# Performance work log

Hardware: AMD Instinct MI355X
Metric: run time of the kernel (lower is better)

The kernel has to match this reference:

```python
import jax, jax.numpy as jnp
import numpy as np

K = 3        # ksize
S = 2        # stride_1
P = K // 2   # padding
SCALE = 10.0 # softmax_scale


def conv1x1(x, w, bias):
    # x: [bs, C, D, H, W], w: [O, C] (1x1x1 Conv3d), bias: [O]
    return jnp.einsum('bcdhw,oc->bodhw', x, w) + bias[None, :, None, None, None]


def _win_idx(n_in):
    n_out = (n_in + 2 * P - K) // S + 1
    idx = (jnp.arange(n_out) * S)[:, None] + jnp.arange(K)  # [n_out, K]
    return idx, n_out


def unfold2d(x):
    # x: [bs, C, H, W] -> patches [bs, C, nH, nW, K, K] (torch Unfold semantics, zero pad)
    bs, C, H, W = x.shape
    xp = jnp.pad(x, ((0, 0), (0, 0), (P, P), (P, P)))
    ri, nH = _win_idx(H)
    ci, nW = _win_idx(W)
    return xp[:, :, ri[:, None, :, None], ci[None, :, None, :]]


def fold2d(pat, H, W):
    # pat: [bs, C, nH, nW, K, K] -> [bs, C, H, W] via overlap-add (torch Fold)
    bs, C, nH, nW, _, _ = pat.shape
    ri, _ = _win_idx(H)
    ci, _ = _win_idx(W)
    out = jnp.zeros((bs, C, H + 2 * P, W + 2 * P), pat.dtype)
    out = out.at[:, :, ri[:, None, :, None], ci[None, :, None, :]].add(pat)
    return out[:, :, P:P + H, P:P + W]


def _patches_flat(x2d):
    # x2d: [bs, Ci, H, W] -> ([bs*L, Ci*K*K], nH, nW)  matching torch's
    # unfold -> view(bs,Ci,K,K,L) -> permute(0,4,1,2,3) -> reshape layout
    pat = unfold2d(x2d)                      # [bs, Ci, nH, nW, K, K]
    bs, Ci, nH, nW = pat.shape[:4]
    flat = jnp.transpose(pat, (0, 2, 3, 1, 4, 5)).reshape(bs * nH * nW, Ci * K * K)
    return flat, nH, nW


def salsa_one(b_one, g_w, g_b, th_w, th_b, ph_w, ph_b, W_w, W_b):
    bs, C, D, H, W = b_one.shape
    Ci = g_w.shape[0]
    b1 = conv1x1(b_one, g_w, g_b)    # query source
    b2 = conv1x1(b_one, th_w, th_b)  # value source
    b3 = conv1x1(b_one, ph_w, ph_b)  # key source
    mid = D // 2

    q, nH, nW = _patches_flat(b1[:, :, mid])   # [bs*L, Ci*K*K]
    v, _, _ = _patches_flat(b2[:, :, mid])
    kq, _, _ = _patches_flat(b3[:, :, mid])

    att = jax.nn.softmax(SCALE * (q @ kq.T), axis=1)  # [bs*L, bs*L]
    zi = att @ v                                      # [bs*L, Ci*K*K]

    pat = jnp.transpose(zi.reshape(bs, nH, nW, Ci, K, K), (0, 3, 1, 2, 4, 5))
    zi2 = fold2d(pat, H, W)                           # [bs, Ci, H, W]
    # overlap-count normalization: fold(unfold(ones))
    mask = fold2d(unfold2d(jnp.ones((bs, Ci, H, W), b_one.dtype)), H, W)
    zi2 = zi2 / mask

    zi5 = jnp.broadcast_to(zi2[:, :, None], (bs, Ci, D, H, W))
    return b_one + conv1x1(zi5, W_w, W_b)


def setup_inputs() -> dict:
    key = jax.random.key(0)
    ks = jax.random.split(key, 9)
    C, Ci = 64, 16
    b = jax.random.normal(ks[0], (2, 1, C, 8, 160, 160), dtype=jnp.float32)
    mk = lambda k, shp: jax.random.normal(k, shp, dtype=jnp.float32) * 0.05
    return {
        'b': b,
        'g_w': mk(ks[1], (Ci, C)), 'g_b': mk(ks[2], (Ci,)),
        'theta_w': mk(ks[3], (Ci, C)), 'theta_b': mk(ks[4], (Ci,)),
        'phi_w': mk(ks[5], (Ci, C)), 'phi_b': mk(ks[6], (Ci,)),
        'W_w': mk(ks[7], (C, Ci)), 'W_b': mk(ks[8], (C,)),
    }


def reference(b, g_w, g_b, theta_w, theta_b, phi_w, phi_b, W_w, W_b):
    f = lambda x: salsa_one(x, g_w, g_b, theta_w, theta_b, phi_w, phi_b, W_w, W_b)
    return jax.vmap(f)(b)
```

## Files before the change

### kernel.cpp

```cpp
#include <hip/hip_runtime.h>


#define NPIX 25600
#define LOG2E10 14.42695040888963f
#define TAU 0.75f

typedef float floatx16 __attribute__((ext_vector_type(16)));
typedef short short8 __attribute__((ext_vector_type(8)));

__device__ inline unsigned short f2bf(float x) {
    union { float f; unsigned int u; } v; v.f = x;
    unsigned int r = v.u + 0x7fffu + ((v.u >> 16) & 1u);
    return (unsigned short)(r >> 16);
}
__device__ inline float bf2f(unsigned short u) {
    union { unsigned int u; float f; } v; v.u = ((unsigned int)u) << 16;
    return v.f;
}

__global__ __launch_bounds__(256) void k_proj(
    const float* __restrict__ b,
    const float* __restrict__ gw, const float* __restrict__ gb,
    const float* __restrict__ thw, const float* __restrict__ thb,
    const float* __restrict__ phw, const float* __restrict__ phb,
    float* __restrict__ P3) {
    __shared__ float Wt[3 * 64 * 16];
    __shared__ float Bl[48];
    __shared__ float red[2][48][64];
    int tid = threadIdx.x;
    int g = blockIdx.y;
    int px = tid & 63;
    int cq = tid >> 6;
    int pix = blockIdx.x * 64 + px;

    for (int i = tid; i < 1024; i += 256) {
        int o = i & 15, c = i >> 4;
        Wt[(0 * 64 + c) * 16 + o] = gw[o * 64 + c];
        Wt[(1 * 64 + c) * 16 + o] = phw[o * 64 + c];
        Wt[(2 * 64 + c) * 16 + o] = thw[o * 64 + c];
    }
    if (tid < 16) { Bl[tid] = gb[tid]; Bl[16 + tid] = phb[tid]; Bl[32 + tid] = thb[tid]; }
    __syncthreads();

    float acc[48];
#pragma unroll
    for (int o = 0; o < 48; o++) acc[o] = 0.f;
    const float* bp = b + (size_t)g * 64 * 8 * NPIX + (size_t)4 * NPIX + pix;
#pragma unroll
    for (int i = 0; i < 16; i++) {
        int c = cq * 16 + i;
        float xv = bp[(size_t)c * 8 * NPIX];
#pragma unroll
        for (int s = 0; s < 3; s++) {
            const float* wp = &Wt[(s * 64 + c) * 16];
#pragma unroll
            for (int o = 0; o < 16; o++)
                acc[s * 16 + o] += wp[o] * xv;
        }
    }
    if (cq >= 2) {
#pragma unroll
        for (int o = 0; o < 48; o++) red[cq - 2][o][px] = acc[o];
    }
    __syncthreads();
    if (cq < 2) {
#pragma unroll
        for (int o = 0; o < 48; o++) acc[o] += red[cq][o][px];
    }
    __syncthreads();
    if (cq == 1) {
#pragma unroll
        for (int o = 0; o < 48; o++) red[0][o][px] = acc[o];
    }
    __syncthreads();
    if (cq == 0) {
#pragma unroll
        for (int o = 0; o < 48; o++)
            P3[(size_t)(g * 48 + o) * NPIX + pix] = acc[o] + red[0][o][px] + Bl[o];
    }
}

__global__ void k_unfold_qk(const float* __restrict__ P3, unsigned short* __restrict__ Pat) {
    int idx = blockIdx.x * 256 + threadIdx.x;
    int f = idx % 144;
    int l = (idx / 144) % 6400;
    int s = (idx / (144 * 6400)) & 1;
    int g = idx / (2 * 144 * 6400);
    int ci = f / 9, kr = (f % 9) / 3, kc = f % 3;
    int oh = l / 80, ow = l % 80;
    int h = oh * 2 + kr - 1, w = ow * 2 + kc - 1;
    float v = 0.f;
    if (h >= 0 && h < 160 && w >= 0 && w < 160)
        v = P3[(size_t)(g * 48 + s * 16 + ci) * NPIX + h * 160 + w];
    Pat[idx] = f2bf(v);
}

__global__ void k_unfold_v(const float* __restrict__ P3, unsigned short* __restrict__ VT) {
    int idx = blockIdx.x * 256 + threadIdx.x;
    int l = idx % 6400;
    int f = (idx / 6400) % 144;
    int g = idx / (144 * 6400);
    int ci = f / 9, kr = (f % 9) / 3, kc = f % 3;
    int oh = l / 80, ow = l % 80;
    int h = oh * 2 + kr - 1, w = ow * 2 + kc - 1;
    float v = 0.f;
    if (h >= 0 && h < 160 && w >= 0 && w < 160)
        v = P3[(size_t)(g * 48 + 32 + ci) * NPIX + h * 160 + w];
    VT[idx] = f2bf(v);
}

__global__ __launch_bounds__(256, 2) void k_attn(
    const unsigned short* __restrict__ PatQK, const unsigned short* __restrict__ VT,
    float* __restrict__ ml, unsigned short* __restrict__ Opart,
    int nsplit, int kps) {
    __shared__ unsigned short Ks[64 * 156];
    __shared__ unsigned short Vs[160 * 76];
    __shared__ unsigned short Pl[4 * 32 * 76];

    int tid = threadIdx.x;
    int lane = tid & 63;
    int w = tid >> 6;
    int l31 = lane & 31;
    int h5 = lane >> 5;
    int split = blockIdx.y, g = blockIdx.z;
    int q = blockIdx.x * 128 + w * 32 + l31;
    int nIter = kps >> 6;

    const unsigned short* Qg = PatQK + ((size_t)g * 2 + 0) * 6400 * 144;
    const unsigned short* Kg = PatQK + ((size_t)g * 2 + 1) * 6400 * 144 + (size_t)split * kps * 144;
    const unsigned short* Vg = VT + (size_t)g * 144 * 6400 + split * kps;

    short8 qf[9];
#pragma unroll
    for (int fs = 0; fs < 9; fs++)
        qf[fs] = *(const short8*)(Qg + (size_t)q * 144 + fs * 16 + h5 * 8);

    floatx16 O[5];
#pragma unroll
    for (int i = 0; i < 5; i++) O[i] = (floatx16)0.f;
    float m = -1e30f, lsum = 0.f;

    unsigned short* Plw = Pl + w * (32 * 76);

    short8 stg[9];
    {
#pragma unroll
        for (int j = 0; j < 9; j++) {
            int c = tid + 256 * j;
            if (c < 1152) {
                int row = c / 18, col = c - row * 18;
                stg[j] = *(const short8*)(Kg + row * 144 + col * 8);
            } else {
                int vv = c - 1152;
                int f = vv >> 3, col = vv & 7;
                stg[j] = *(const short8*)(Vg + (size_t)f * 6400 + col * 8);
            }
        }
#pragma unroll
        for (int j = 0; j < 9; j++) {
            int c = tid + 256 * j;
            if (c < 1152) {
                int row = c / 18, col = c - row * 18;
                *(short8*)&Ks[row * 156 + col * 8] = stg[j];
            } else {
                int vv = c - 1152;
                int f = vv >> 3, col = vv & 7;
                *(short8*)&Vs[f * 76 + col * 8] = stg[j];
            }
        }
    }

    for (int it = 0; it < nIter; it++) {
        __syncthreads();

        if (it + 1 < nIter) {
            const unsigned short* Kt = Kg + (it + 1) * 64 * 144;
            const unsigned short* Vt = Vg + (it + 1) * 64;
#pragma unroll
            for (int j = 0; j < 9; j++) {
                int c = tid + 256 * j;
                if (c < 1152) {
                    int row = c / 18, col = c - row * 18;
                    stg[j] = *(const short8*)(Kt + row * 144 + col * 8);
                } else {
                    int vv = c - 1152;
                    int f = vv >> 3, col = vv & 7;
                    stg[j] = *(const short8*)(Vt + (size_t)f * 6400 + col * 8);
                }
            }
        }

        floatx16 S0 = (floatx16)0.f, S1 = (floatx16)0.f;
#pragma unroll
        for (int fs = 0; fs < 9; fs++) {
            short8 a0 = *(const short8*)&Ks[l31 * 156 + fs * 16 + h5 * 8];
            short8 a1 = *(const short8*)&Ks[(32 + l31) * 156 + fs * 16 + h5 * 8];
            S0 = __builtin_amdgcn_mfma_f32_32x32x16_bf16(a0, qf[fs], S0, 0, 0, 0);
            S1 = __builtin_amdgcn_mfma_f32_32x32x16_bf16(a1, qf[fs], S1, 0, 0, 0);
        }

        float mt = -1e30f;
#pragma unroll
        for (int r = 0; r < 16; r++) { mt = fmaxf(mt, S0[r]); mt = fmaxf(mt, S1[r]); }
        mt = fmaxf(mt, __shfl_xor(mt, 32, 64));
        bool upd = mt > m + TAU;
        float mnew = upd ? mt : m;
        float alpha = upd ? exp2f(LOG2E10 * (m - mnew)) : 1.f;
        float ps = 0.f;
#pragma unroll
        for (int r = 0; r < 16; r++) {
            S0[r] = exp2f(LOG2E10 * (S0[r] - mnew));
            S1[r] = exp2f(LOG2E10 * (S1[r] - mnew));
            ps += S0[r] + S1[r];
        }
        ps += __shfl_xor(ps, 32, 64);
        lsum = lsum * alpha + ps;
        m = mnew;
        if (__any(alpha < 1.f)) {
#pragma unroll
            for (int t5 = 0; t5 < 5; t5++)
#pragma unroll
                for (int r = 0; r < 16; r++) O[t5][r] *= alpha;
        }

#pragma unroll
        for (int rg = 0; rg < 4; rg++) {
            ushort4 w0, w1;
            w0.x = f2bf(S0[4 * rg + 0]); w0.y = f2bf(S0[4 * rg + 1]);
            w0.z = f2bf(S0[4 * rg + 2]); w0.w = f2bf(S0[4 * rg + 3]);
            w1.x = f2bf(S1[4 * rg + 0]); w1.y = f2bf(S1[4 * rg + 1]);
            w1.z = f2bf(S1[4 * rg + 2]); w1.w = f2bf(S1[4 * rg + 3]);
            *(ushort4*)&Plw[l31 * 76 + rg * 8 + h5 * 4] = w0;
            *(ushort4*)&Plw[l31 * 76 + 32 + rg * 8 + h5 * 4] = w1;
        }

#pragma unroll
        for (int ks = 0; ks < 4; ks++) {
            short8 pb = *(const short8*)&Plw[l31 * 76 + ks * 16 + h5 * 8];
#pragma unroll
            for (int ft = 0; ft < 5; ft++) {
                short8 va = *(const short8*)&Vs[(ft * 32 + l31) * 76 + ks * 16 + h5 * 8];
                O[ft] = __builtin_amdgcn_mfma_f32_32x32x16_bf16(va, pb, O[ft], 0, 0, 0);
            }
        }

        __syncthreads();
        if (it + 1 < nIter) {
#pragma unroll
            for (int j = 0; j < 9; j++) {
                int c = tid + 256 * j;
                if (c < 1152) {
                    int row = c / 18, col = c - row * 18;
                    *(short8*)&Ks[row * 156 + col * 8] = stg[j];
                } else {
                    int vv = c - 1152;
                    int f = vv >> 3, col = vv & 7;
                    *(short8*)&Vs[f * 76 + col * 8] = stg[j];
                }
            }
        }
    }

    if (h5 == 0)
        ((float2*)ml)[((size_t)g * nsplit + split) * 6400 + q] = make_float2(m, lsum);

    unsigned short* Og = Opart + (((size_t)g * nsplit + split) * 6400 + q) * 144;
#pragma unroll
    for (int ft = 0; ft < 5; ft++)
#pragma unroll
        for (int rg = 0; rg < 4; rg++) {
            int f = ft * 32 + rg * 8 + h5 * 4;
            if (f < 144) {
                ushort4 st;
                st.x = f2bf(O[ft][4 * rg + 0]); st.y = f2bf(O[ft][4 * rg + 1]);
                st.z = f2bf(O[ft][4 * rg + 2]); st.w = f2bf(O[ft][4 * rg + 3]);
                *(ushort4*)(Og + f) = st;
            }
        }
}

__global__ void k_merge(const float* __restrict__ mlp, const unsigned short* __restrict__ Opart,
                        float* __restrict__ Zi, int nsplit) {
    int idx = blockIdx.x * 256 + threadIdx.x;
    int fg = idx % 36;
    int q = (idx / 36) % 6400;
    int g = idx / (36 * 6400);
    const float2* ml2 = (const float2*)mlp;
    float2 s[5];
    float ms = -1e30f;
#pragma unroll
    for (int k = 0; k < 5; k++) {
        s[k] = (k < nsplit) ? ml2[((size_t)g * nsplit + k) * 6400 + q]
                            : make_float2(-1e30f, 0.f);
        ms = fmaxf(ms, s[k].x);
    }
    float wgt[5], denom = 0.f;
#pragma unroll
    for (int k = 0; k < 5; k++) {
        wgt[k] = exp2f(LOG2E10 * (s[k].x - ms));
        denom += wgt[k] * s[k].y;
    }
    float inv = 1.f / denom;
    float a0 = 0.f, a1 = 0.f, a2 = 0.f, a3 = 0.f;
#pragma unroll
    for (int k = 0; k < 5; k++) {
        if (k < nsplit) {
            ushort4 u = *(const ushort4*)(Opart + (((size_t)g * nsplit + k) * 6400 + q) * 144 + fg * 4);
            a0 += wgt[k] * bf2f(u.x); a1 += wgt[k] * bf2f(u.y);
            a2 += wgt[k] * bf2f(u.z); a3 += wgt[k] * bf2f(u.w);
        }
    }
    float4 out = make_float4(a0 * inv, a1 * inv, a2 * inv, a3 * inv);
    *(float4*)(Zi + ((size_t)g * 6400 + q) * 144 + fg * 4) = out;
}

__global__ void k_fold(const float* __restrict__ Zi, float* __restrict__ zi2) {
    int idx = blockIdx.x * 256 + threadIdx.x;
    int pix = idx % NPIX;
    int ci = (idx / NPIX) & 15;
    int g = idx / (16 * NPIX);
    int h = pix / 160, w = pix % 160;
    int ohs[2], krs[2], nh = 0;
#pragma unroll
    for (int kr = 0; kr < 3; kr++) {
        int t = h + 1 - kr;
        if (t >= 0 && (t & 1) == 0 && (t >> 1) < 80) { ohs[nh] = t >> 1; krs[nh] = kr; nh++; }
    }
    int ows[2], kcs[2], nw = 0;
#pragma unroll
    for (int kc = 0; kc < 3; kc++) {
        int t = w + 1 - kc;
        if (t >= 0 && (t & 1) == 0 && (t >> 1) < 80) { ows[nw] = t >> 1; kcs[nw] = kc; nw++; }
    }
    float sm = 0.f;
    for (int a = 0; a < nh; a++)
        for (int bb = 0; bb < nw; bb++) {
            int l = ohs[a] * 80 + ows[bb];
            int f = ci * 9 + krs[a] * 3 + kcs[bb];
            sm += Zi[((size_t)g * 6400 + l) * 144 + f];
        }
    zi2[idx] = sm / (float)(nh * nw);
}

__global__ void k_final(const float* __restrict__ b, const float* __restrict__ zi2,
                        const float* __restrict__ Ww, const float* __restrict__ Wb,
                        float* __restrict__ out) {
    __shared__ float z[16 * 64];
    __shared__ float Wl[64 * 16];
    __shared__ float Bl[64];
    int tid = threadIdx.x;
    int g = blockIdx.y;
    int pxb = blockIdx.x * 64;
    for (int i = tid; i < 1024; i += 256) {
        int ci = i >> 6, px = i & 63;
        z[i] = zi2[(size_t)(g * 16 + ci) * NPIX + pxb + px];
        Wl[i] = Ww[i];
    }
    if (tid < 64) Bl[tid] = Wb[tid];
    __syncthreads();

    int px4 = tid & 15;
    int cg = tid >> 4;
    float acc[4][4];
#pragma unroll
    for (int c4 = 0; c4 < 4; c4++) {
        float bv = Bl[cg + 16 * c4];
#pragma unroll
        for (int j = 0; j < 4; j++) acc[c4][j] = bv;
    }
#pragma unroll
    for (int ci = 0; ci < 16; ci++) {
        float zv[4];
#pragma unroll
        for (int j = 0; j < 4; j++) zv[j] = z[ci * 64 + px4 * 4 + j];
#pragma unroll
        for (int c4 = 0; c4 < 4; c4++) {
            float wv = Wl[(cg + 16 * c4) * 16 + ci];
#pragma unroll
            for (int j = 0; j < 4; j++) acc[c4][j] += wv * zv[j];
        }
    }
    for (int d = 0; d < 8; d++) {
#pragma unroll
        for (int c4 = 0; c4 < 4; c4++) {
            int c = cg + 16 * c4;
            size_t base = ((size_t)(g * 64 + c) * 8 + d) * NPIX + pxb + px4 * 4;
            float4 bv = *(const float4*)(b + base);
            float4 ov = make_float4(bv.x + acc[c4][0], bv.y + acc[c4][1],
                                    bv.z + acc[c4][2], bv.w + acc[c4][3]);
            *(float4*)(out + base) = ov;
        }
    }
}

extern "C" void kernel_launch(void* const* d_in, const int* in_sizes, int n_in,
                              void* d_out, int out_size, void* d_ws, size_t ws_size,
                              hipStream_t stream) {
    const float* b   = (const float*)d_in[0];
    const float* gw  = (const float*)d_in[1];
    const float* gb  = (const float*)d_in[2];
    const float* thw = (const float*)d_in[3];
    const float* thb = (const float*)d_in[4];
    const float* phw = (const float*)d_in[5];
    const float* phb = (const float*)d_in[6];
    const float* Ww  = (const float*)d_in[7];
    const float* Wb  = (const float*)d_in[8];
    float* out = (float*)d_out;
    float* ws = (float*)d_ws;

    const size_t need5 = 30003200;
    int ns = (ws_size >= need5) ? 5 : 4;
    int kps = 6400 / ns;

    unsigned short* PatQK = (unsigned short*)ws;
    unsigned short* VT    = (unsigned short*)(ws + 1843200);
    float*          ml    = ws + 2764800;
    size_t off_P3 = 2764800 + (size_t)2 * ns * 6400 * 2;
    float*          P3    = ws + off_P3;
    unsigned short* Opart = (unsigned short*)(ws + off_P3);
    float*          Zi    = ws;
    float*          zi2   = ws + 1843200;

    k_proj<<<dim3(400, 2), 256, 0, stream>>>(b, gw, gb, thw, thb, phw, phb, P3);
    k_unfold_qk<<<dim3(14400), 256, 0, stream>>>(P3, PatQK);
    k_unfold_v<<<dim3(7200), 256, 0, stream>>>(P3, VT);
    k_attn<<<dim3(50, ns, 2), 256, 0, stream>>>(PatQK, VT, ml, Opart, ns, kps);
    k_merge<<<dim3(1800), 256, 0, stream>>>(ml, Opart, Zi, ns);
    k_fold<<<dim3(3200), 256, 0, stream>>>(Zi, zi2);
    k_final<<<dim3(400, 2), 256, 0, stream>>>(b, zi2, Ww, Wb, out);
}
```

Before: 344.0 us.

## Shrink attention LDS footprint, alias P buffer over K, raise occupancy and splits

The attention kernel now keeps K and V in one shared buffer with tighter padding, and reuses the K region for the per-wave probability tile. This needs an extra barrier after the score computation. Launch bounds ask for 4 blocks per CU instead of 2, and the key dimension is split 10 ways when the workspace allows it, with the merge kernel extended to match. The aim is more resident waves and more blocks to hide latency. The costs are register pressure that may cause spills, an extra sync per iteration, more partial outputs to merge, and possible bank conflicts from the new strides.

```diff
diff --git a/kernel.cpp b/kernel.cpp
--- a/kernel.cpp
+++ b/kernel.cpp
@@ -4,6 +4,12 @@
 #define NPIX 25600
 #define LOG2E10 14.42695040888963f
 #define TAU 0.75f
+
+#define KS_LD 146
+#define VS_LD 66
+#define PL_LD 66
+#define KS_SH (64 * KS_LD)
+#define VS_SH (160 * VS_LD)
 
 typedef float floatx16 __attribute__((ext_vector_type(16)));
 typedef short short8 __attribute__((ext_vector_type(8)));
@@ -109,13 +115,14 @@
     VT[idx] = f2bf(v);
 }
 
-__global__ __launch_bounds__(256, 2) void k_attn(
+__global__ __launch_bounds__(256, 4) void k_attn(
     const unsigned short* __restrict__ PatQK, const unsigned short* __restrict__ VT,
     float* __restrict__ ml, unsigned short* __restrict__ Opart,
     int nsplit, int kps) {
-    __shared__ unsigned short Ks[64 * 156];
-    __shared__ unsigned short Vs[160 * 76];
-    __shared__ unsigned short Pl[4 * 32 * 76];
+    __shared__ unsigned short SM[KS_SH + VS_SH];
+    unsigned short* Ks = SM;
+    unsigned short* Vs = SM + KS_SH;
+    unsigned short* Pl = SM;
 
     int tid = threadIdx.x;
     int lane = tid & 63;
@@ -140,7 +147,9 @@
     for (int i = 0; i < 5; i++) O[i] = (floatx16)0.f;
     float m = -1e30f, lsum = 0.f;
 
-    unsigned short* Plw = Pl + w * (32 * 76);
+    unsigned short* Plw = Pl + w * (32 * PL_LD);
+
+    for (int i = tid; i < 16 * VS_LD; i += 256) Vs[144 * VS_LD + i] = 0;
 
     short8 stg[9];
     {
@@ -161,11 +170,11 @@
             int c = tid + 256 * j;
             if (c < 1152) {
                 int row = c / 18, col = c - row * 18;
-                *(short8*)&Ks[row * 156 + col * 8] = stg[j];
+                *(short8*)&Ks[row * KS_LD + col * 8] = stg[j];
             } else {
                 int vv = c - 1152;
                 int f = vv >> 3, col = vv & 7;
-                *(short8*)&Vs[f * 76 + col * 8] = stg[j];
+                *(short8*)&Vs[f * VS_LD + col * 8] = stg[j];
             }
         }
     }
@@ -193,8 +202,8 @@
         floatx16 S0 = (floatx16)0.f, S1 = (floatx16)0.f;
 #pragma unroll
         for (int fs = 0; fs < 9; fs++) {
-            short8 a0 = *(const short8*)&Ks[l31 * 156 + fs * 16 + h5 * 8];
-            short8 a1 = *(const short8*)&Ks[(32 + l31) * 156 + fs * 16 + h5 * 8];
+            short8 a0 = *(const short8*)&Ks[l31 * KS_LD + fs * 16 + h5 * 8];
+            short8 a1 = *(const short8*)&Ks[(32 + l31) * KS_LD + fs * 16 + h5 * 8];
             S0 = __builtin_amdgcn_mfma_f32_32x32x16_bf16(a0, qf[fs], S0, 0, 0, 0);
             S1 = __builtin_amdgcn_mfma_f32_32x32x16_bf16(a1, qf[fs], S1, 0, 0, 0);
         }
@@ -223,6 +232,8 @@
                 for (int r = 0; r < 16; r++) O[t5][r] *= alpha;
         }
 
+        __syncthreads();
+
 #pragma unroll
         for (int rg = 0; rg < 4; rg++) {
             ushort4 w0, w1;
@@ -230,32 +241,32 @@
             w0.z = f2bf(S0[4 * rg + 2]); w0.w = f2bf(S0[4 * rg + 3]);
             w1.x = f2bf(S1[4 * rg + 0]); w1.y = f2bf(S1[4 * rg + 1]);
             w1.z = f2bf(S1[4 * rg + 2]); w1.w = f2bf(S1[4 * rg + 3]);
-            *(ushort4*)&Plw[l31 * 76 + rg * 8 + h5 * 4] = w0;
-            *(ushort4*)&Plw[l31 * 76 + 32 + rg * 8 + h5 * 4] = w1;
+            *(ushort4*)&Plw[l31 * PL_LD + rg * 8 + h5 * 4] = w0;
+            *(ushort4*)&Plw[l31 * PL_LD + 32 + rg * 8 + h5 * 4] = w1;
         }
 
 #pragma unroll
         for (int ks = 0; ks < 4; ks++) {
-            short8 pb = *(const short8*)&Plw[l31 * 76 + ks * 16 + h5 * 8];
+            short8 pb = *(const short8*)&Plw[l31 * PL_LD + ks * 16 + h5 * 8];
 #pragma unroll
             for (int ft = 0; ft < 5; ft++) {
-                short8 va = *(const short8*)&Vs[(ft * 32 + l31) * 76 + ks * 16 + h5 * 8];
+                short8 va = *(const short8*)&Vs[(ft * 32 + l31) * VS_LD + ks * 16 + h5 * 8];
                 O[ft] = __builtin_amdgcn_mfma_f32_32x32x16_bf16(va, pb, O[ft], 0, 0, 0);
             }
         }
 
-        __syncthreads();
         if (it + 1 < nIter) {
+            __syncthreads();
 #pragma unroll
             for (int j = 0; j < 9; j++) {
                 int c = tid + 256 * j;
                 if (c < 1152) {
                     int row = c / 18, col = c - row * 18;
-                    *(short8*)&Ks[row * 156 + col * 8] = stg[j];
+                    *(short8*)&Ks[row * KS_LD + col * 8] = stg[j];
                 } else {
                     int vv = c - 1152;
                     int f = vv >> 3, col = vv & 7;
-                    *(short8*)&Vs[f * 76 + col * 8] = stg[j];
+                    *(short8*)&Vs[f * VS_LD + col * 8] = stg[j];
                 }
             }
         }
@@ -286,24 +297,24 @@
     int q = (idx / 36) % 6400;
     int g = idx / (36 * 6400);
     const float2* ml2 = (const float2*)mlp;
-    float2 s[5];
+    float2 s[10];
     float ms = -1e30f;
 #pragma unroll
-    for (int k = 0; k < 5; k++) {
+    for (int k = 0; k < 10; k++) {
         s[k] = (k < nsplit) ? ml2[((size_t)g * nsplit + k) * 6400 + q]
                             : make_float2(-1e30f, 0.f);
         ms = fmaxf(ms, s[k].x);
     }
-    float wgt[5], denom = 0.f;
-#pragma unroll
-    for (int k = 0; k < 5; k++) {
+    float wgt[10], denom = 0.f;
+#pragma unroll
+    for (int k = 0; k < 10; k++) {
         wgt[k] = exp2f(LOG2E10 * (s[k].x - ms));
         denom += wgt[k] * s[k].y;
     }
     float inv = 1.f / denom;
     float a0 = 0.f, a1 = 0.f, a2 = 0.f, a3 = 0.f;
 #pragma unroll
-    for (int k = 0; k < 5; k++) {
+    for (int k = 0; k < 10; k++) {
         if (k < nsplit) {
             ushort4 u = *(const ushort4*)(Opart + (((size_t)g * nsplit + k) * 6400 + q) * 144 + fg * 4);
             a0 += wgt[k] * bf2f(u.x); a1 += wgt[k] * bf2f(u.y);
@@ -408,8 +419,9 @@
     float* out = (float*)d_out;
     float* ws = (float*)d_ws;
 
-    const size_t need5 = 30003200;
-    int ns = (ws_size >= need5) ? 5 : 4;
+    const size_t need10 = 48947200;
+    const size_t need5  = 30003200;
+    int ns = (ws_size >= need10) ? 10 : (ws_size >= need5) ? 5 : 4;
     int kps = 6400 / ns;
 
     unsigned short* PatQK = (unsigned short*)ws;
```

Result: slower. 591.3 us (+71.9%).
